# Performance work log

Measured on AMD Instinct MI355X. Metric: run time of the kernel, lower is better.

Reference implementation:

```python
import jax, jax.numpy as jnp
import numpy as np

SCALING = 2.0

def setup_inputs() -> dict:
    key = jax.random.key(0)
    k1, k2 = jax.random.split(key)
    N, C, D, H, W = 8, 64, 16, 128, 128
    x = jax.random.normal(k1, (N, C, D, H, W), dtype=jnp.float32)
    bias = jax.random.normal(k2, (C,), dtype=jnp.float32)
    return {"x": x, "bias": bias}

def reference(x, bias):
    # x: [N,C,D,H,W] -> mean over depth D -> [N,C,H,W]
    logits = jnp.mean(x, axis=2) + bias[None, :, None, None]
    # channel-wise numerically-stable softmax over C (axis=1)
    p = jax.nn.softmax(logits, axis=1)
    return jnp.tanh(p) * SCALING
```

## Files before the change

kernel.cpp:

```cpp
#include <hip/hip_runtime.h>

constexpr int C     = 64;
constexpr int D     = 16;
constexpr int HW    = 128 * 128;
constexpr int HW4   = HW / 4;
constexpr int STILE = 256;
constexpr float SCALING = 2.0f;

__global__ __launch_bounds__(512, 4) void fused_lds_v5(
    const float* __restrict__ x,
    const float* __restrict__ bias,
    float* __restrict__ out)
{
    __shared__ float logit[C][STILE];
    __shared__ float red[2][STILE];

    const int b      = blockIdx.x;
    const int n      = b >> 6;
    const int s_base = (b & 63) * STILE;

    const int q = threadIdx.x & 63;
    const int g = threadIdx.x >> 6;

    #pragma unroll
    for (int k = 0; k < 8; ++k) {
        const int c = g * 8 + k;
        const float4* p =
            (const float4*)(x + ((size_t)(n * C + c) * D) * HW + s_base) + q;
        float4 a0 = {0, 0, 0, 0}, a1 = a0, a2 = a0, a3 = a0;
        #pragma unroll
        for (int d = 0; d < D; d += 4) {
            float4 v0 = p[(size_t)(d + 0) * HW4];
            float4 v1 = p[(size_t)(d + 1) * HW4];
            float4 v2 = p[(size_t)(d + 2) * HW4];
            float4 v3 = p[(size_t)(d + 3) * HW4];
            a0.x += v0.x; a0.y += v0.y; a0.z += v0.z; a0.w += v0.w;
            a1.x += v1.x; a1.y += v1.y; a1.z += v1.z; a1.w += v1.w;
            a2.x += v2.x; a2.y += v2.y; a2.z += v2.z; a2.w += v2.w;
            a3.x += v3.x; a3.y += v3.y; a3.z += v3.z; a3.w += v3.w;
        }
        const float bc = bias[c];
        float4 r;
        r.x = ((a0.x + a1.x) + (a2.x + a3.x)) * (1.0f / D) + bc;
        r.y = ((a0.y + a1.y) + (a2.y + a3.y)) * (1.0f / D) + bc;
        r.z = ((a0.z + a1.z) + (a2.z + a3.z)) * (1.0f / D) + bc;
        r.w = ((a0.w + a1.w) + (a2.w + a3.w)) * (1.0f / D) + bc;
        *(float4*)&logit[c][4 * q] = r;
    }
    __syncthreads();

    const int s     = threadIdx.x & 255;
    const int h     = threadIdx.x >> 8;
    const int cbase = h * 32;

    float mine[32];
    float sum = 0.f;
    #pragma unroll
    for (int k = 0; k < 32; ++k) {
        const float e = __expf(logit[cbase + k][s]);
        mine[k] = e;
        sum += e;
    }
    red[h][s] = sum;
    __syncthreads();
    const float inv = 1.0f / (red[0][s] + red[1][s]);

    float* po = out + (size_t)(n * C + cbase) * HW + s_base + s;
    #pragma unroll
    for (int k = 0; k < 32; ++k) {
        const float pv = mine[k] * inv;
        const float e  = __expf(2.0f * pv);
        po[(size_t)k * HW] = SCALING * (1.0f - 2.0f / (e + 1.0f));
    }
}

extern "C" void kernel_launch(void* const* d_in, const int* in_sizes, int n_in,
                              void* d_out, int out_size, void* d_ws, size_t ws_size,
                              hipStream_t stream)
{
    const float* x    = (const float*)d_in[0];
    const float* bias = (const float*)d_in[1];
    float* out        = (float*)d_out;

    const int N      = in_sizes[0] / (C * D * HW);
    const int blocks = N * (HW / STILE);
    fused_lds_v5<<<blocks, 512, 0, stream>>>(x, bias, out);
}
```

Measured before the change: 111.4 us.

## Keep softmax exponentials in registers and use nontemporal vector loads/stores

Each thread now keeps its own 8 channels x 4 pixels of exponentials in registers and does the channel reduction through a small LDS partial-sum array, instead of staging all logits in a 64KB LDS tile and re-reading them by a different thread mapping. This drops the large LDS footprint and one of the two barriers, and the output is written as float4 nontemporal stores. Input loads are also marked nontemporal to avoid cache pollution on streamed data. The kernel is dominated by reading 537MB, so the gain depends mostly on whether nontemporal hints and higher occupancy help DRAM throughput.

```diff
diff --git a/kernel.cpp b/kernel.cpp
--- a/kernel.cpp
+++ b/kernel.cpp
@@ -1,4 +1,6 @@
 #include <hip/hip_runtime.h>
+
+typedef float f32x4 __attribute__((ext_vector_type(4)));
 
 constexpr int C     = 64;
 constexpr int D     = 16;
@@ -7,13 +9,12 @@
 constexpr int STILE = 256;
 constexpr float SCALING = 2.0f;
 
-__global__ __launch_bounds__(512, 4) void fused_lds_v5(
+__global__ __launch_bounds__(512, 4) void fused_reg_v6(
     const float* __restrict__ x,
     const float* __restrict__ bias,
     float* __restrict__ out)
 {
-    __shared__ float logit[C][STILE];
-    __shared__ float red[2][STILE];
+    __shared__ f32x4 red4[8][64];
 
     const int b      = blockIdx.x;
     const int n      = b >> 6;
@@ -22,55 +23,51 @@
     const int q = threadIdx.x & 63;
     const int g = threadIdx.x >> 6;
 
+    f32x4 mine[8];
     #pragma unroll
     for (int k = 0; k < 8; ++k) {
         const int c = g * 8 + k;
-        const float4* p =
-            (const float4*)(x + ((size_t)(n * C + c) * D) * HW + s_base) + q;
-        float4 a0 = {0, 0, 0, 0}, a1 = a0, a2 = a0, a3 = a0;
+        const f32x4* p =
+            (const f32x4*)(x + ((size_t)(n * C + c) * D) * HW + s_base) + q;
+        f32x4 a0 = {0, 0, 0, 0}, a1 = a0, a2 = a0, a3 = a0;
         #pragma unroll
         for (int d = 0; d < D; d += 4) {
-            float4 v0 = p[(size_t)(d + 0) * HW4];
-            float4 v1 = p[(size_t)(d + 1) * HW4];
-            float4 v2 = p[(size_t)(d + 2) * HW4];
-            float4 v3 = p[(size_t)(d + 3) * HW4];
-            a0.x += v0.x; a0.y += v0.y; a0.z += v0.z; a0.w += v0.w;
-            a1.x += v1.x; a1.y += v1.y; a1.z += v1.z; a1.w += v1.w;
-            a2.x += v2.x; a2.y += v2.y; a2.z += v2.z; a2.w += v2.w;
-            a3.x += v3.x; a3.y += v3.y; a3.z += v3.z; a3.w += v3.w;
+            a0 += __builtin_nontemporal_load(p + (size_t)(d + 0) * HW4);
+            a1 += __builtin_nontemporal_load(p + (size_t)(d + 1) * HW4);
+            a2 += __builtin_nontemporal_load(p + (size_t)(d + 2) * HW4);
+            a3 += __builtin_nontemporal_load(p + (size_t)(d + 3) * HW4);
         }
-        const float bc = bias[c];
-        float4 r;
-        r.x = ((a0.x + a1.x) + (a2.x + a3.x)) * (1.0f / D) + bc;
-        r.y = ((a0.y + a1.y) + (a2.y + a3.y)) * (1.0f / D) + bc;
-        r.z = ((a0.z + a1.z) + (a2.z + a3.z)) * (1.0f / D) + bc;
-        r.w = ((a0.w + a1.w) + (a2.w + a3.w)) * (1.0f / D) + bc;
-        *(float4*)&logit[c][4 * q] = r;
+        f32x4 r = ((a0 + a1) + (a2 + a3)) * (1.0f / D) + bias[c];
+        f32x4 e;
+        e.x = __expf(r.x); e.y = __expf(r.y);
+        e.z = __expf(r.z); e.w = __expf(r.w);
+        mine[k] = e;
     }
+
+    f32x4 ps = ((mine[0] + mine[1]) + (mine[2] + mine[3]))
+             + ((mine[4] + mine[5]) + (mine[6] + mine[7]));
+    red4[g][q] = ps;
     __syncthreads();
 
-    const int s     = threadIdx.x & 255;
-    const int h     = threadIdx.x >> 8;
-    const int cbase = h * 32;
+    f32x4 tot = red4[0][q];
+    #pragma unroll
+    for (int j = 1; j < 8; ++j) tot += red4[j][q];
+    f32x4 inv;
+    inv.x = 1.0f / tot.x; inv.y = 1.0f / tot.y;
+    inv.z = 1.0f / tot.z; inv.w = 1.0f / tot.w;
 
-    float mine[32];
-    float sum = 0.f;
+    float* po = out + (size_t)(n * C + g * 8) * HW + s_base + 4 * q;
     #pragma unroll
-    for (int k = 0; k < 32; ++k) {
-        const float e = __expf(logit[cbase + k][s]);
-        mine[k] = e;
-        sum += e;
-    }
-    red[h][s] = sum;
-    __syncthreads();
-    const float inv = 1.0f / (red[0][s] + red[1][s]);
-
-    float* po = out + (size_t)(n * C + cbase) * HW + s_base + s;
-    #pragma unroll
-    for (int k = 0; k < 32; ++k) {
-        const float pv = mine[k] * inv;
-        const float e  = __expf(2.0f * pv);
-        po[(size_t)k * HW] = SCALING * (1.0f - 2.0f / (e + 1.0f));
+    for (int k = 0; k < 8; ++k) {
+        f32x4 pv = mine[k] * inv;
+        f32x4 e2, r;
+        e2.x = __expf(2.0f * pv.x); e2.y = __expf(2.0f * pv.y);
+        e2.z = __expf(2.0f * pv.z); e2.w = __expf(2.0f * pv.w);
+        r.x = SCALING * (1.0f - 2.0f / (e2.x + 1.0f));
+        r.y = SCALING * (1.0f - 2.0f / (e2.y + 1.0f));
+        r.z = SCALING * (1.0f - 2.0f / (e2.z + 1.0f));
+        r.w = SCALING * (1.0f - 2.0f / (e2.w + 1.0f));
+        __builtin_nontemporal_store(r, (f32x4*)(po + (size_t)k * HW));
     }
 }
 
@@ -84,5 +81,5 @@
 
     const int N      = in_sizes[0] / (C * D * HW);
     const int blocks = N * (HW / STILE);
-    fused_lds_v5<<<blocks, 512, 0, stream>>>(x, bias, out);
+    fused_reg_v6<<<blocks, 512, 0, stream>>>(x, bias, out);
 }
```

Result: faster. 95.49 us, median of 2 (-14.3%).
